# Optimization experiments

Hardware: AMD Instinct MI355X
Metric: run time of the kernel (lower is better)

The kernel has to match this reference:

```python
import jax, jax.numpy as jnp
import numpy as np

NUM_EMBEDDINGS = 1024
EMBEDDING_DIM = 256


def setup_inputs() -> dict:
    key = jax.random.key(0)
    k1, k2 = jax.random.split(key)
    z = jax.random.normal(k1, (32, EMBEDDING_DIM, 32, 32), dtype=jnp.float32)
    codebook = jax.random.normal(k2, (NUM_EMBEDDINGS, EMBEDDING_DIM), dtype=jnp.float32)
    return {"z": z, "codebook": codebook}


def reference(z, codebook):
    # z: (B, C, H, W) -> (B, H, W, C) -> (B*H*W, C)
    B, C, H, W = z.shape
    z_bhwc = jnp.transpose(z, (0, 2, 3, 1))
    z_flat = z_bhwc.reshape(-1, C)  # (N, C)

    # pairwise squared distances: ||z||^2 + ||e||^2 - 2 z.e^T  -> (N, K)
    distances = (
        jnp.sum(z_flat ** 2, axis=1, keepdims=True)
        + jnp.sum(codebook ** 2, axis=1)
        - 2.0 * jnp.matmul(z_flat, codebook.T)
    )
    argmin_codewords = jnp.argmin(distances, axis=1)  # (N,)
    min_codewords = jax.nn.one_hot(argmin_codewords, NUM_EMBEDDINGS, dtype=jnp.float32)  # (N, K)

    # quantized latents via one-hot @ codebook, back to (B, C, H, W)
    z_quantized = jnp.matmul(min_codewords, codebook).reshape(B, H, W, C)
    z_quantized = jnp.transpose(z_quantized, (0, 3, 1, 2))
    return (min_codewords, z_quantized)
```

## Files before the change

kernel.cpp:

```cpp
#include <hip/hip_runtime.h>

#define N_ROWS 32768
#define K_CODES 1024
#define CDIM 256

typedef _Float16 half8 __attribute__((ext_vector_type(8)));
typedef _Float16 half4 __attribute__((ext_vector_type(4)));
typedef float floatx16 __attribute__((ext_vector_type(16)));
typedef unsigned long long ull;

#define WS_ZH   0ull
#define WS_ZL   16777216ull
#define WS_CBH  33554432ull
#define WS_CBL  34078720ull
#define WS_CBN  34603008ull
#define WS_PART 34607104ull
#define WS_IDX  36704256ull
#define WS_NEED 36835328ull

__device__ __forceinline__ void g2lds16(const void* g, void* l) {
    __builtin_amdgcn_global_load_lds(
        (const __attribute__((address_space(1))) void*)g,
        (__attribute__((address_space(3))) void*)l, 16, 0, 0);
}


__global__ __launch_bounds__(64) void cb_prep(const float* __restrict__ cb,
                                              _Float16* __restrict__ cbh,
                                              _Float16* __restrict__ cbl,
                                              float* __restrict__ cbn) {
    int k = blockIdx.x;
    int lane = threadIdx.x;
    float4 v = reinterpret_cast<const float4*>(cb + k * CDIM)[lane];
    float s0 = v.x * 32.f, s1 = v.y * 32.f, s2 = v.z * 32.f, s3 = v.w * 32.f;
    half4 hv, lv;
    hv[0] = (_Float16)s0; lv[0] = (_Float16)(s0 - (float)hv[0]);
    hv[1] = (_Float16)s1; lv[1] = (_Float16)(s1 - (float)hv[1]);
    hv[2] = (_Float16)s2; lv[2] = (_Float16)(s2 - (float)hv[2]);
    hv[3] = (_Float16)s3; lv[3] = (_Float16)(s3 - (float)hv[3]);
    int cc = lane >> 3;
    int q  = (lane >> 1) & 3;
    size_t off = (size_t)((cc * 4 + q) * K_CODES + k) * 8 + (lane & 1) * 4;
    *reinterpret_cast<half4*>(&cbh[off]) = hv;
    *reinterpret_cast<half4*>(&cbl[off]) = lv;
    float s = s0 * s0 + s1 * s1 + s2 * s2 + s3 * s3;
    #pragma unroll
    for (int off2 = 32; off2 > 0; off2 >>= 1) s += __shfl_down(s, off2);
    if (lane == 0) cbn[k] = s;
}

__global__ __launch_bounds__(256) void z_prep(const float* __restrict__ z,
                                              _Float16* __restrict__ zh,
                                              _Float16* __restrict__ zl) {
    __shared__ float t[64][68];
    int hwt = blockIdx.x & 15;
    int ct  = (blockIdx.x >> 4) & 3;
    int bb  = blockIdx.x >> 6;
    int tid = threadIdx.x;
    #pragma unroll
    for (int p = 0; p < 4; p++) {
        int e = p * 256 + tid;
        int c = e >> 4, h4 = e & 15;
        float4 v = *reinterpret_cast<const float4*>(
            &z[((bb * 256 + ct * 64 + c) << 10) + hwt * 64 + h4 * 4]);
        *reinterpret_cast<float4*>(&t[c][h4 * 4]) = v;
    }
    __syncthreads();
    int hw = tid & 63, g8 = tid >> 6;
    int n = bb * 1024 + hwt * 64 + hw;
    #pragma unroll
    for (int p = 0; p < 2; p++) {
        int o = g8 * 2 + p;
        int cg = ct * 64 + o * 8;
        int cc = cg >> 5, q = (cg >> 3) & 3;
        half8 hv, lv;
        #pragma unroll
        for (int j = 0; j < 8; j++) {
            float s = t[o * 8 + j][hw] * 32.f;
            _Float16 h = (_Float16)s;
            hv[j] = h;
            lv[j] = (_Float16)(s - (float)h);
        }
        size_t off = (size_t)((cc * 4 + q) * N_ROWS + n) * 8;
        *reinterpret_cast<half8*>(&zh[off]) = hv;
        *reinterpret_cast<half8*>(&zl[off]) = lv;
    }
}

__global__ __launch_bounds__(256, 4) void vq_mfma32(
    const _Float16* __restrict__ zh, const _Float16* __restrict__ zl,
    const _Float16* __restrict__ cbh, const _Float16* __restrict__ cbl,
    const float* __restrict__ cbn, ull* __restrict__ partial) {

    __shared__ _Float16 AhL[4096], AlL[4096];
    __shared__ _Float16 BhL[4096], BlL[4096];

    const int tid = threadIdx.x;
    const int lane = tid & 63, wave = tid >> 6;
    const int wm = wave & 1, wn = wave >> 1;
    const int fm = lane & 31, fq = lane >> 5;
    const int codeTile = blockIdx.x >> 8;
    const int g = blockIdx.x & 255;
    const int rowTile = (g & 7) * 32 + (g >> 3);
    const int rowBase = rowTile * 128, codeBase = codeTile * 128;

    floatx16 acc[4];
    #pragma unroll
    for (int i = 0; i < 4; i++) acc[i] = (floatx16)0.f;

    for (int kc = 0; kc < CDIM; kc += 32) {
        const int cc = kc >> 5;
        #pragma unroll
        for (int i = 0; i < 2; i++) {
            int G = i * 256 + tid;
            int q = G >> 7, r = G & 127;
            size_t so = (size_t)((cc * 4 + q) * N_ROWS + rowBase + r) * 8;
            g2lds16(zh + so, &AhL[G * 8]);
            g2lds16(zl + so, &AlL[G * 8]);
        }
        #pragma unroll
        for (int i = 0; i < 2; i++) {
            int G = i * 256 + tid;
            int q = G >> 7, c2 = G & 127;
            size_t so = (size_t)((cc * 4 + q) * K_CODES + codeBase + c2) * 8;
            g2lds16(cbh + so, &BhL[G * 8]);
            g2lds16(cbl + so, &BlL[G * 8]);
        }
        __syncthreads();
        #pragma unroll
        for (int s = 0; s < 2; s++) {
            int q = s * 2 + fq;
            half8 ah[2], al[2], bh[2], bl[2];
            #pragma unroll
            for (int i = 0; i < 2; i++) {
                int ga = q * 128 + wm * 64 + i * 32 + fm;
                ah[i] = *reinterpret_cast<const half8*>(&AhL[ga * 8]);
                al[i] = *reinterpret_cast<const half8*>(&AlL[ga * 8]);
            }
            #pragma unroll
            for (int j = 0; j < 2; j++) {
                int gb = q * 128 + wn * 64 + j * 32 + fm;
                bh[j] = *reinterpret_cast<const half8*>(&BhL[gb * 8]);
                bl[j] = *reinterpret_cast<const half8*>(&BlL[gb * 8]);
            }
            #pragma unroll
            for (int i = 0; i < 2; i++)
                #pragma unroll
                for (int j = 0; j < 2; j++) {
                    acc[i*2+j] = __builtin_amdgcn_mfma_f32_32x32x16_f16(ah[i], bh[j], acc[i*2+j], 0, 0, 0);
                    acc[i*2+j] = __builtin_amdgcn_mfma_f32_32x32x16_f16(al[i], bh[j], acc[i*2+j], 0, 0, 0);
                    acc[i*2+j] = __builtin_amdgcn_mfma_f32_32x32x16_f16(ah[i], bl[j], acc[i*2+j], 0, 0, 0);
                }
        }
        __syncthreads();
    }

    float (*rvv)[2] = reinterpret_cast<float(*)[2]>(&AhL[0]);
    int   (*rcc)[2] = reinterpret_cast<int(*)[2]>(&AhL[1024]);

    float cbnv[2];
    #pragma unroll
    for (int j = 0; j < 2; j++) cbnv[j] = cbn[codeBase + wn * 64 + j * 32 + fm];

    #pragma unroll
    for (int i = 0; i < 2; i++)
        #pragma unroll
        for (int r = 0; r < 16; r++) {
            float best = 3.4e38f; int bcode = 0x7fffffff;
            #pragma unroll
            for (int j = 0; j < 2; j++) {
                float d = fmaf(-2.f, acc[i*2+j][r], cbnv[j]);
                int code = codeBase + wn * 64 + j * 32 + fm;
                if (d < best) { best = d; bcode = code; }
            }
            #pragma unroll
            for (int m = 1; m < 32; m <<= 1) {
                float ov = __shfl_xor(best, m, 64);
                int   oc = __shfl_xor(bcode, m, 64);
                if (ov < best || (ov == best && oc < bcode)) { best = ov; bcode = oc; }
            }
            if (fm == 0) {
                int row = wm * 64 + i * 32 + (r & 3) + 8 * (r >> 2) + 4 * fq;
                rvv[row][wn] = best;
                rcc[row][wn] = bcode;
            }
        }
    __syncthreads();
    if (tid < 128) {
        float v0 = rvv[tid][0]; int c0 = rcc[tid][0];
        float v1 = rvv[tid][1]; int c1 = rcc[tid][1];
        if (v1 < v0 || (v1 == v0 && c1 < c0)) { v0 = v1; c0 = c1; }
        unsigned u = __float_as_uint(v0);
        u = (u & 0x80000000u) ? ~u : (u | 0x80000000u);
        partial[(size_t)(rowBase + tid) * 8 + codeTile] =
            ((ull)u << 32) | (unsigned)c0;
    }
}

__global__ __launch_bounds__(256) void onehot_fin(const ull* __restrict__ partial,
                                                  int* __restrict__ idx,
                                                  float* __restrict__ out) {
    int row = blockIdx.x;
    __shared__ int sid;
    if (threadIdx.x < 64) {
        ull v = (threadIdx.x < 8) ? partial[(size_t)row * 8 + threadIdx.x]
                                  : ~0ull;
        #pragma unroll
        for (int m = 1; m < 8; m <<= 1) {
            ull o = __shfl_xor(v, m, 64);
            if (o < v) v = o;
        }
        if (threadIdx.x == 0) {
            int id = (int)(v & 0xffffffffu);
            sid = id;
            idx[row] = id;
        }
    }
    __syncthreads();
    int id = sid;
    int k4 = threadIdx.x << 2;
    float4 v4;
    v4.x = (k4     == id) ? 1.f : 0.f;
    v4.y = (k4 + 1 == id) ? 1.f : 0.f;
    v4.z = (k4 + 2 == id) ? 1.f : 0.f;
    v4.w = (k4 + 3 == id) ? 1.f : 0.f;
    reinterpret_cast<float4*>(out)[(size_t)row * 256 + threadIdx.x] = v4;
}

__global__ __launch_bounds__(256) void zq_fill(const int* __restrict__ idx,
                                               const float* __restrict__ cb,
                                               float* __restrict__ out) {
    int i  = blockIdx.x * 256 + threadIdx.x;
    int hw = i & 1023;
    int c  = (i >> 10) & 255;
    int b  = i >> 18;
    int n  = (b << 10) | hw;
    out[i] = cb[idx[n] * CDIM + c];
}


__global__ __launch_bounds__(64) void cb_norms(const float* __restrict__ cb,
                                               float* __restrict__ cbn) {
    int k = blockIdx.x;
    int lane = threadIdx.x;
    float4 v = reinterpret_cast<const float4*>(cb + k * CDIM)[lane];
    float s = v.x * v.x + v.y * v.y + v.z * v.z + v.w * v.w;
    #pragma unroll
    for (int off = 32; off > 0; off >>= 1) s += __shfl_down(s, off);
    if (lane == 0) cbn[k] = s;
}

__global__ __launch_bounds__(256) void cb_transpose(const float* __restrict__ cb,
                                                    float* __restrict__ cbt) {
    __shared__ float t[32][33];
    int k0 = (blockIdx.x & 31) * 32;
    int c0 = (blockIdx.x >> 5) * 32;
    int lane = threadIdx.x & 31;
    int row = threadIdx.x >> 5;
    #pragma unroll
    for (int s = 0; s < 4; s++) {
        int r = row + s * 8;
        t[r][lane] = cb[(k0 + r) * CDIM + c0 + lane];
    }
    __syncthreads();
    #pragma unroll
    for (int s = 0; s < 4; s++) {
        int r = row + s * 8;
        cbt[(c0 + r) * K_CODES + k0 + lane] = t[lane][r];
    }
}

__global__ __launch_bounds__(512, 2) void vq_argmin(const float* __restrict__ z,
                                                    const float* __restrict__ cbt,
                                                    const float* __restrict__ cbn,
                                                    int* __restrict__ idx_out) {
    __shared__ float As[64][128];
    __shared__ float Bs[64][256];

    const int tid = threadIdx.x;
    const int tx = tid & 31;
    const int ty = tid >> 5;
    const int rowBase = blockIdx.x * 128;
    const int bb = rowBase >> 10;
    const int hwBase = rowBase & 1023;

    float minv[8];
    int   mini[8];
    #pragma unroll
    for (int i = 0; i < 8; i++) { minv[i] = 3.4e38f; mini[i] = 0; }

    for (int kt = 0; kt < K_CODES; kt += 256) {
        float acc[2][2][4][4];
        #pragma unroll
        for (int a = 0; a < 2; a++)
            #pragma unroll
            for (int b = 0; b < 2; b++)
                #pragma unroll
                for (int i = 0; i < 4; i++)
                    #pragma unroll
                    for (int j = 0; j < 4; j++) acc[a][b][i][j] = 0.f;

        for (int ccb = 0; ccb < CDIM; ccb += 64) {
            #pragma unroll
            for (int l = 0; l < 4; l++) {
                int f = tid + l * 512;
                int r4 = f & 31, c = f >> 5;
                float4 v = *reinterpret_cast<const float4*>(
                    &z[((bb * 256 + ccb + c) << 10) + hwBase + r4 * 4]);
                *reinterpret_cast<float4*>(&As[c][r4 * 4]) = v;
            }
            #pragma unroll
            for (int l = 0; l < 8; l++) {
                int f = tid + l * 512;
                int k4 = f & 63, c = f >> 6;
                float4 v = *reinterpret_cast<const float4*>(
                    &cbt[(ccb + c) * K_CODES + kt + k4 * 4]);
                *reinterpret_cast<float4*>(&Bs[c][k4 * 4]) = v;
            }
            __syncthreads();
            #pragma unroll 4
            for (int c = 0; c < 64; c++) {
                float4 a0 = *reinterpret_cast<const float4*>(&As[c][ty * 4]);
                float4 a1 = *reinterpret_cast<const float4*>(&As[c][64 + ty * 4]);
                float4 b0 = *reinterpret_cast<const float4*>(&Bs[c][tx * 4]);
                float4 b1 = *reinterpret_cast<const float4*>(&Bs[c][128 + tx * 4]);
                float av[2][4] = {{a0.x, a0.y, a0.z, a0.w}, {a1.x, a1.y, a1.z, a1.w}};
                float bw[2][4] = {{b0.x, b0.y, b0.z, b0.w}, {b1.x, b1.y, b1.z, b1.w}};
                #pragma unroll
                for (int ri = 0; ri < 2; ri++)
                    #pragma unroll
                    for (int i = 0; i < 4; i++)
                        #pragma unroll
                        for (int ci = 0; ci < 2; ci++)
                            #pragma unroll
                            for (int j = 0; j < 4; j++)
                                acc[ri][ci][i][j] =
                                    fmaf(av[ri][i], bw[ci][j], acc[ri][ci][i][j]);
            }
            __syncthreads();
        }
        #pragma unroll
        for (int ci = 0; ci < 2; ci++)
            #pragma unroll
            for (int j = 0; j < 4; j++) {
                int code = kt + ci * 128 + tx * 4 + j;
                float nrm = cbn[code];
                #pragma unroll
                for (int ri = 0; ri < 2; ri++)
                    #pragma unroll
                    for (int i = 0; i < 4; i++) {
                        float d = fmaf(-2.f, acc[ri][ci][i][j], nrm);
                        int r = ri * 4 + i;
                        if (d < minv[r]) { minv[r] = d; mini[r] = code; }
                    }
            }
    }

    __syncthreads();
    float (*rv)[32] = reinterpret_cast<float(*)[32]>(&As[0][0]);
    int   (*rix)[32] = reinterpret_cast<int(*)[32]>(&As[32][0]);
    #pragma unroll
    for (int ri = 0; ri < 2; ri++)
        #pragma unroll
        for (int i = 0; i < 4; i++) {
            int row = ri * 64 + ty * 4 + i;
            rv[row][tx] = minv[ri * 4 + i];
            rix[row][tx] = mini[ri * 4 + i];
        }
    __syncthreads();
    if (tid < 128) {
        float bvv = rv[tid][0]; int bii = rix[tid][0];
        #pragma unroll
        for (int t = 1; t < 32; t++) {
            float v = rv[tid][t]; int ii = rix[tid][t];
            if (v < bvv || (v == bvv && ii < bii)) { bvv = v; bii = ii; }
        }
        idx_out[rowBase + tid] = bii;
    }
}

__global__ __launch_bounds__(256) void onehot_fill(const int* __restrict__ idx,
                                                   float* __restrict__ out) {
    int i = blockIdx.x * 256 + threadIdx.x;
    int n  = i >> 8;
    int k4 = (i & 255) << 2;
    int id = idx[n];
    float4 v;
    v.x = (k4     == id) ? 1.f : 0.f;
    v.y = (k4 + 1 == id) ? 1.f : 0.f;
    v.z = (k4 + 2 == id) ? 1.f : 0.f;
    v.w = (k4 + 3 == id) ? 1.f : 0.f;
    reinterpret_cast<float4*>(out)[i] = v;
}

extern "C" void kernel_launch(void* const* d_in, const int* in_sizes, int n_in,
                              void* d_out, int out_size, void* d_ws, size_t ws_size,
                              hipStream_t stream) {
    const float* z  = (const float*)d_in[0];
    const float* cb = (const float*)d_in[1];
    float* out0 = (float*)d_out;
    float* out1 = out0 + (size_t)N_ROWS * K_CODES;

    if (ws_size >= WS_NEED) {
        _Float16* zh  = (_Float16*)((char*)d_ws + WS_ZH);
        _Float16* zl  = (_Float16*)((char*)d_ws + WS_ZL);
        _Float16* cbh = (_Float16*)((char*)d_ws + WS_CBH);
        _Float16* cbl = (_Float16*)((char*)d_ws + WS_CBL);
        float* cbn = (float*)((char*)d_ws + WS_CBN);
        ull* part = (ull*)((char*)d_ws + WS_PART);
        int* idx = (int*)((char*)d_ws + WS_IDX);

        cb_prep<<<K_CODES, 64, 0, stream>>>(cb, cbh, cbl, cbn);
        z_prep<<<2048, 256, 0, stream>>>(z, zh, zl);
        vq_mfma32<<<2048, 256, 0, stream>>>(zh, zl, cbh, cbl, cbn, part);
        onehot_fin<<<N_ROWS, 256, 0, stream>>>(part, idx, out0);
        zq_fill<<<(N_ROWS * CDIM) / 256, 256, 0, stream>>>(idx, cb, out1);
    } else {
        float* cbn = (float*)d_ws;
        int*   idx = (int*)((char*)d_ws + 4096);
        float* cbt = (float*)((char*)d_ws + 4096 + 131072);

        cb_norms<<<K_CODES, 64, 0, stream>>>(cb, cbn);
        cb_transpose<<<256, 256, 0, stream>>>(cb, cbt);
        vq_argmin<<<N_ROWS / 128, 512, 0, stream>>>(z, cbt, cbn, idx);
        onehot_fill<<<(N_ROWS * K_CODES / 4) / 256, 256, 0, stream>>>(idx, out0);
        zq_fill<<<(N_ROWS * CDIM) / 256, 256, 0, stream>>>(idx, cb, out1);
    }
}
```

Measured before the change: 303.6 us.

## Triple-buffer LDS loads in VQ MFMA kernel with async waitcnt pipelining

The distance GEMM kernel now stages 16-channel K slices through a 3-deep LDS ring buffer. The next slice is issued with global_load_lds before computing the current one, and each step uses a vmcnt wait plus a single barrier instead of two __syncthreads per step. The layout index math in the prep kernels is simplified to a flat ccq index, which produces the same addresses. Occupancy hint drops from 4 to 3 blocks per CU to fit the larger LDS footprint. This trades occupancy for overlap of global loads with MFMA work, and the barrier-per-step scheme relies on the three-buffer distance to avoid overwrite races.

```diff
diff --git a/kernel.cpp b/kernel.cpp
--- a/kernel.cpp
+++ b/kernel.cpp
@@ -23,6 +23,9 @@
         (const __attribute__((address_space(1))) void*)g,
         (__attribute__((address_space(3))) void*)l, 16, 0, 0);
 }
+
+#define WAITCNT_VM4() __builtin_amdgcn_s_waitcnt(4 | (7 << 4) | (15 << 8))
+#define WAITCNT_VM0() __builtin_amdgcn_s_waitcnt(0 | (7 << 4) | (15 << 8))
 
 
 __global__ __launch_bounds__(64) void cb_prep(const float* __restrict__ cb,
@@ -38,9 +41,8 @@
     hv[1] = (_Float16)s1; lv[1] = (_Float16)(s1 - (float)hv[1]);
     hv[2] = (_Float16)s2; lv[2] = (_Float16)(s2 - (float)hv[2]);
     hv[3] = (_Float16)s3; lv[3] = (_Float16)(s3 - (float)hv[3]);
-    int cc = lane >> 3;
-    int q  = (lane >> 1) & 3;
-    size_t off = (size_t)((cc * 4 + q) * K_CODES + k) * 8 + (lane & 1) * 4;
+    int ccq = lane >> 1;
+    size_t off = (size_t)(ccq * K_CODES + k) * 8 + (lane & 1) * 4;
     *reinterpret_cast<half4*>(&cbh[off]) = hv;
     *reinterpret_cast<half4*>(&cbl[off]) = lv;
     float s = s0 * s0 + s1 * s1 + s2 * s2 + s3 * s3;
@@ -71,8 +73,7 @@
     #pragma unroll
     for (int p = 0; p < 2; p++) {
         int o = g8 * 2 + p;
-        int cg = ct * 64 + o * 8;
-        int cc = cg >> 5, q = (cg >> 3) & 3;
+        int ccq = (ct * 64 + o * 8) >> 3;
         half8 hv, lv;
         #pragma unroll
         for (int j = 0; j < 8; j++) {
@@ -81,19 +82,19 @@
             hv[j] = h;
             lv[j] = (_Float16)(s - (float)h);
         }
-        size_t off = (size_t)((cc * 4 + q) * N_ROWS + n) * 8;
+        size_t off = (size_t)(ccq * N_ROWS + n) * 8;
         *reinterpret_cast<half8*>(&zh[off]) = hv;
         *reinterpret_cast<half8*>(&zl[off]) = lv;
     }
 }
 
-__global__ __launch_bounds__(256, 4) void vq_mfma32(
+__global__ __launch_bounds__(256, 3) void vq_pipe(
     const _Float16* __restrict__ zh, const _Float16* __restrict__ zl,
     const _Float16* __restrict__ cbh, const _Float16* __restrict__ cbl,
     const float* __restrict__ cbn, ull* __restrict__ partial) {
 
-    __shared__ _Float16 AhL[4096], AlL[4096];
-    __shared__ _Float16 BhL[4096], BlL[4096];
+    __shared__ _Float16 AhL[3][2048], AlL[3][2048];
+    __shared__ _Float16 BhL[3][2048], BlL[3][2048];
 
     const int tid = threadIdx.x;
     const int lane = tid & 63, wave = tid >> 6;
@@ -104,59 +105,69 @@
     const int rowTile = (g & 7) * 32 + (g >> 3);
     const int rowBase = rowTile * 128, codeBase = codeTile * 128;
 
+    const int sq = tid >> 7, sr = tid & 127;
+    const size_t aBase = (size_t)(rowBase + sr) * 8;
+    const size_t bBase = (size_t)(codeBase + sr) * 8;
+
     floatx16 acc[4];
     #pragma unroll
     for (int i = 0; i < 4; i++) acc[i] = (floatx16)0.f;
 
-    for (int kc = 0; kc < CDIM; kc += 32) {
-        const int cc = kc >> 5;
+    {
+        size_t soA = (size_t)(sq * N_ROWS) * 8 + aBase;
+        size_t soB = (size_t)(sq * K_CODES) * 8 + bBase;
+        int d = (sq * 128 + sr) * 8;
+        g2lds16(zh + soA,  &AhL[0][d]);
+        g2lds16(zl + soA,  &AlL[0][d]);
+        g2lds16(cbh + soB, &BhL[0][d]);
+        g2lds16(cbl + soB, &BlL[0][d]);
+    }
+
+    #pragma unroll
+    for (int k = 0; k < 16; k++) {
+        const int cbuf = k % 3;
+        if (k < 15) {
+            const int nbuf = (k + 1) % 3;
+            const int ccq = 2 * (k + 1) + sq;
+            size_t soA = (size_t)(ccq * N_ROWS) * 8 + aBase;
+            size_t soB = (size_t)(ccq * K_CODES) * 8 + bBase;
+            int d = (sq * 128 + sr) * 8;
+            g2lds16(zh + soA,  &AhL[nbuf][d]);
+            g2lds16(zl + soA,  &AlL[nbuf][d]);
+            g2lds16(cbh + soB, &BhL[nbuf][d]);
+            g2lds16(cbl + soB, &BlL[nbuf][d]);
+            WAITCNT_VM4();
+        } else {
+            WAITCNT_VM0();
+        }
+        __builtin_amdgcn_s_barrier();
+
+        half8 ah[2], al[2], bh[2], bl[2];
         #pragma unroll
         for (int i = 0; i < 2; i++) {
-            int G = i * 256 + tid;
-            int q = G >> 7, r = G & 127;
-            size_t so = (size_t)((cc * 4 + q) * N_ROWS + rowBase + r) * 8;
-            g2lds16(zh + so, &AhL[G * 8]);
-            g2lds16(zl + so, &AlL[G * 8]);
-        }
-        #pragma unroll
-        for (int i = 0; i < 2; i++) {
-            int G = i * 256 + tid;
-            int q = G >> 7, c2 = G & 127;
-            size_t so = (size_t)((cc * 4 + q) * K_CODES + codeBase + c2) * 8;
-            g2lds16(cbh + so, &BhL[G * 8]);
-            g2lds16(cbl + so, &BlL[G * 8]);
-        }
-        __syncthreads();
-        #pragma unroll
-        for (int s = 0; s < 2; s++) {
-            int q = s * 2 + fq;
-            half8 ah[2], al[2], bh[2], bl[2];
-            #pragma unroll
-            for (int i = 0; i < 2; i++) {
-                int ga = q * 128 + wm * 64 + i * 32 + fm;
-                ah[i] = *reinterpret_cast<const half8*>(&AhL[ga * 8]);
-                al[i] = *reinterpret_cast<const half8*>(&AlL[ga * 8]);
-            }
+            int ga = (fq * 128 + wm * 64 + i * 32 + fm) * 8;
+            ah[i] = *reinterpret_cast<const half8*>(&AhL[cbuf][ga]);
+            al[i] = *reinterpret_cast<const half8*>(&AlL[cbuf][ga]);
+        }
+        #pragma unroll
+        for (int j = 0; j < 2; j++) {
+            int gb = (fq * 128 + wn * 64 + j * 32 + fm) * 8;
+            bh[j] = *reinterpret_cast<const half8*>(&BhL[cbuf][gb]);
+            bl[j] = *reinterpret_cast<const half8*>(&BlL[cbuf][gb]);
+        }
+        #pragma unroll
+        for (int i = 0; i < 2; i++)
             #pragma unroll
             for (int j = 0; j < 2; j++) {
-                int gb = q * 128 + wn * 64 + j * 32 + fm;
-                bh[j] = *reinterpret_cast<const half8*>(&BhL[gb * 8]);
-                bl[j] = *reinterpret_cast<const half8*>(&BlL[gb * 8]);
-            }
-            #pragma unroll
-            for (int i = 0; i < 2; i++)
-                #pragma unroll
-                for (int j = 0; j < 2; j++) {
-                    acc[i*2+j] = __builtin_amdgcn_mfma_f32_32x32x16_f16(ah[i], bh[j], acc[i*2+j], 0, 0, 0);
-                    acc[i*2+j] = __builtin_amdgcn_mfma_f32_32x32x16_f16(al[i], bh[j], acc[i*2+j], 0, 0, 0);
-                    acc[i*2+j] = __builtin_amdgcn_mfma_f32_32x32x16_f16(ah[i], bl[j], acc[i*2+j], 0, 0, 0);
-                }
-        }
-        __syncthreads();
-    }
-
-    float (*rvv)[2] = reinterpret_cast<float(*)[2]>(&AhL[0]);
-    int   (*rcc)[2] = reinterpret_cast<int(*)[2]>(&AhL[1024]);
+                acc[i*2+j] = __builtin_amdgcn_mfma_f32_32x32x16_f16(ah[i], bh[j], acc[i*2+j], 0, 0, 0);
+                acc[i*2+j] = __builtin_amdgcn_mfma_f32_32x32x16_f16(al[i], bh[j], acc[i*2+j], 0, 0, 0);
+                acc[i*2+j] = __builtin_amdgcn_mfma_f32_32x32x16_f16(ah[i], bl[j], acc[i*2+j], 0, 0, 0);
+            }
+    }
+    __syncthreads();
+
+    float (*rvv)[2] = reinterpret_cast<float(*)[2]>(&AhL[0][0]);
+    int   (*rcc)[2] = reinterpret_cast<int(*)[2]>(&AhL[0][1024]);
 
     float cbnv[2];
     #pragma unroll
@@ -412,7 +423,7 @@
 
         cb_prep<<<K_CODES, 64, 0, stream>>>(cb, cbh, cbl, cbn);
         z_prep<<<2048, 256, 0, stream>>>(z, zh, zl);
-        vq_mfma32<<<2048, 256, 0, stream>>>(zh, zl, cbh, cbl, cbn, part);
+        vq_pipe<<<2048, 256, 0, stream>>>(zh, zl, cbh, cbl, cbn, part);
         onehot_fin<<<N_ROWS, 256, 0, stream>>>(part, idx, out0);
         zq_fill<<<(N_ROWS * CDIM) / 256, 256, 0, stream>>>(idx, cb, out1);
     } else {
```

Result: slower. 315.2 us (+3.8%).
